# Kernel tuning notes

Hardware: AMD Instinct MI355X
Metric: run time of the kernel (lower is better)

Reference implementation:

```python
import jax, jax.numpy as jnp
import numpy as np


def squash(t, axis=0):
    # torch: norm over `axis` (dim removed), then norm^2 * t / ((1+norm^2)*norm),
    # broadcasting the reduced norm against t (right-aligned broadcast).
    norm = jnp.linalg.norm(t, axis=axis)
    return (norm ** 2) * t / ((1.0 + norm ** 2) * norm)


def setup_inputs() -> dict:
    key = jax.random.key(0)
    k1, k2 = jax.random.split(key)
    x = jax.random.normal(k1, (8, 16, 96, 96), dtype=jnp.float32)
    # (ker_h=5, ker_w=5, in_maps=16, num_atoms=8, out_maps=16)
    weights = jax.random.normal(k2, (5, 5, 16, 8, 16), dtype=jnp.float32)
    return {"x": x, "weights": weights, "num_routes": 3}


def reference(x, weights, num_routes):
    B, Cin, H, W = x.shape
    kh, kw, _, A, Cout = weights.shape

    # --- voting: zero-insertion (x2) + pad 2 + 5x5 sliding windows + einsum ---
    # torch builds a 2Hx2W zero-inserted tensor (trailing zero row/col), pads by 2,
    # then unfolds 5x5 patches at every position -> output spatial 2H x 2W and
    # contracts 'abcdef,efbhi->acdhi' (cross-correlation over kernel + in_maps).
    # This is exactly an lhs-dilated conv: dilation 2 gives size 2H-1, so pad
    # (2, 3) reproduces the torch layout (pad 2 each side of 2H incl. trailing zero).
    w = weights.reshape(kh, kw, Cin, A * Cout)  # HWIO
    out = jax.lax.conv_general_dilated(
        x, w,
        window_strides=(1, 1),
        padding=[(2, 3), (2, 3)],
        lhs_dilation=(2, 2),
        dimension_numbers=("NCHW", "HWIO", "NHWC"),
    )  # (B, 2H, 2W, A*Cout)
    votes = out.reshape(B, 2 * H, 2 * W, A, Cout)      # acdhi
    votes = jnp.transpose(votes, (0, 3, 4, 1, 2))      # (B, A, Cout, 2H, 2W) = abcde

    # --- dynamic routing (faithful, incl. softmax over the BATCH axis and the
    # logits = softmax(logits) reassignment before the additive update) ---
    logits = jnp.zeros((B, A, 2 * H, 2 * W), dtype=x.dtype)
    preds = None
    for _ in range(num_routes):
        logits = jax.nn.softmax(logits, axis=0)
        preds = jnp.einsum("abcde,abde->bcde", votes, logits)  # sum over batch
        preds = squash(preds, axis=0)                            # over num_atoms
        logits = logits + jnp.einsum("abcde,bcde->abde", votes, preds)
    return preds  # (A, Cout, 2H, 2W)
```

## Files before the change

kernel.cpp:

```cpp
#include <hip/hip_runtime.h>

#define XH 96
#define XW 96
#define CIN 16
#define NA 8
#define NC 16
#define OH 192
#define OW 192
#define WP 102
#define PADN (CIN * XH * WP * 8)

__global__ __launch_bounds__(256) void pad_x(const float* __restrict__ x,
                                             float* __restrict__ xp) {
  int idx = blockIdx.x * 256 + threadIdx.x;
  if (idx >= PADN) return;
  int b   = idx & 7;
  int t   = idx >> 3;
  int ixp = t % WP;
  int t2  = t / WP;
  int iy  = t2 % XH;
  int ci  = t2 / XH;
  int ix  = ixp - 1;
  float v = 0.f;
  if (ix >= 0 && ix < XW)
    v = x[((b * CIN + ci) * XH + iy) * XW + ix];
  xp[idx] = v;
}

__device__ __forceinline__ void route_pair(
    const float (&va)[8][2], const float (&vb)[8][2],
    int R, float (&qa)[2], float (&qb)[2])
{
  float lga[8], lgb[8];
#pragma unroll
  for (int b = 0; b < 8; ++b) { lga[b] = 0.f; lgb[b] = 0.f; }
#pragma unroll 1
  for (int r = 0; r < R; ++r) {
    float sla[8], slb[8];
    if (r == 0) {
#pragma unroll
      for (int b = 0; b < 8; ++b) { sla[b] = 0.125f; slb[b] = 0.125f; }
    } else {
      float ma = lga[0], mb = lgb[0];
#pragma unroll
      for (int b = 1; b < 8; ++b) { ma = fmaxf(ma, lga[b]); mb = fmaxf(mb, lgb[b]); }
      float sa = 0.f, sb = 0.f;
#pragma unroll
      for (int b = 0; b < 8; ++b) {
        sla[b] = __expf(lga[b] - ma); sa += sla[b];
        slb[b] = __expf(lgb[b] - mb); sb += slb[b];
      }
      const float ira = __builtin_amdgcn_rcpf(sa);
      const float irb = __builtin_amdgcn_rcpf(sb);
#pragma unroll
      for (int b = 0; b < 8; ++b) { sla[b] *= ira; slb[b] *= irb; }
    }

    qa[0] = 0.f; qa[1] = 0.f; qb[0] = 0.f; qb[1] = 0.f;
#pragma unroll
    for (int b = 0; b < 8; ++b) {
      qa[0] += va[b][0] * sla[b];  qa[1] += va[b][1] * sla[b];
      qb[0] += vb[b][0] * slb[b];  qb[1] += vb[b][1] * slb[b];
    }

#pragma unroll
    for (int i = 0; i < 2; ++i) {
      float na = qa[i] * qa[i], nb = qb[i] * qb[i];
      na += __shfl_xor(na, 8);  nb += __shfl_xor(nb, 8);
      na += __shfl_xor(na, 16); nb += __shfl_xor(nb, 16);
      na += __shfl_xor(na, 32); nb += __shfl_xor(nb, 32);
      qa[i] *= sqrtf(na) * __builtin_amdgcn_rcpf(1.f + na);
      qb[i] *= sqrtf(nb) * __builtin_amdgcn_rcpf(1.f + nb);
    }

    if (r + 1 < R) {
#pragma unroll
      for (int b = 0; b < 8; ++b) {
        float da = va[b][0] * qa[0] + va[b][1] * qa[1];
        float db = vb[b][0] * qb[0] + vb[b][1] * qb[1];
        da += __shfl_xor(da, 1);  db += __shfl_xor(db, 1);
        da += __shfl_xor(da, 2);  db += __shfl_xor(db, 2);
        da += __shfl_xor(da, 4);  db += __shfl_xor(db, 4);
        lga[b] = sla[b] + da;     lgb[b] = slb[b] + db;
      }
    }
  }
}

__global__ __launch_bounds__(256, 4) void upcaps_tr(
    const float* __restrict__ xp,
    const float* __restrict__ wts,
    const int* __restrict__ nroutes,
    float* __restrict__ out)
{
  __shared__ float lds_out[16 * 128];

  const int lane = threadIdx.x & 63;
  const int wid  = threadIdx.x >> 6;
  const int tile = blockIdx.x;
  const int oy   = tile / 12;
  const int xg   = (tile - oy * 12) * 16;
  const int pxb  = (wid & 1) + ((wid >> 1) << 3);
  const int oxw  = xg + pxb;
  const int a    = lane >> 3;
  const int cg   = lane & 7;
  const int e    = oxw & 1;
  const int ixp0 = __builtin_amdgcn_readfirstlane(((oxw - 2 + e) >> 1) + 1);
  const bool use_t2 = (__builtin_amdgcn_readfirstlane(e) == 0);
  const int wlane = a * NC + cg * 2;

  float acc[4][8][2];
#pragma unroll
  for (int j = 0; j < 4; ++j)
#pragma unroll
    for (int b = 0; b < 8; ++b) { acc[j][b][0] = 0.f; acc[j][b][1] = 0.f; }

  for (int ky = 0; ky < 5; ++ky) {
    const int py = oy - 2 + ky;
    if (py < 0 || py > 2 * XH - 2 || (py & 1)) continue;
    const int iy = py >> 1;
#pragma unroll 2
    for (int ci = 0; ci < CIN; ++ci) {
      const float* xrow = xp + ((ci * XH + iy) * WP + ixp0) * 8;
      float2 wv0, wv1, wv2;
      {
        const float* w0 = wts + ((ky * 5 + e)     * CIN + ci) * (NA * NC) + wlane;
        const float* w1 = wts + ((ky * 5 + e + 2) * CIN + ci) * (NA * NC) + wlane;
        wv0 = *(const float2*)w0;
        wv1 = *(const float2*)w1;
        wv2 = make_float2(0.f, 0.f);
        if (use_t2) {
          const float* w2 = wts + ((ky * 5 + 4) * CIN + ci) * (NA * NC) + wlane;
          wv2 = *(const float2*)w2;
        }
      }
#pragma unroll
      for (int ir = 0; ir < 6; ++ir) {
        if (ir == 5 && !use_t2) continue;
        const float4 xlo = *(const float4*)(xrow + ir * 8);
        const float4 xhi = *(const float4*)(xrow + ir * 8 + 4);
        const float xv[8] = {xlo.x, xlo.y, xlo.z, xlo.w,
                             xhi.x, xhi.y, xhi.z, xhi.w};
        if (ir <= 3) {
#pragma unroll
          for (int b = 0; b < 8; ++b) {
            acc[ir][b][0] += xv[b] * wv0.x;  acc[ir][b][1] += xv[b] * wv0.y;
          }
        }
        if (ir >= 1 && ir <= 4) {
#pragma unroll
          for (int b = 0; b < 8; ++b) {
            acc[ir-1][b][0] += xv[b] * wv1.x;  acc[ir-1][b][1] += xv[b] * wv1.y;
          }
        }
        if (ir >= 2 && use_t2) {
#pragma unroll
          for (int b = 0; b < 8; ++b) {
            acc[ir-2][b][0] += xv[b] * wv2.x;  acc[ir-2][b][1] += xv[b] * wv2.y;
          }
        }
      }
    }
  }

  const int R = nroutes[0];
  float q0[2], q1[2], q2[2], q3[2];
  route_pair(acc[0], acc[1], R, q0, q1);
  route_pair(acc[2], acc[3], R, q2, q3);

  const int lbase = a * NC + cg * 2;
  *(float2*)&lds_out[(pxb    ) * 128 + lbase] = make_float2(q0[0], q0[1]);
  *(float2*)&lds_out[(pxb + 2) * 128 + lbase] = make_float2(q1[0], q1[1]);
  *(float2*)&lds_out[(pxb + 4) * 128 + lbase] = make_float2(q2[0], q2[1]);
  *(float2*)&lds_out[(pxb + 6) * 128 + lbase] = make_float2(q3[0], q3[1]);
  __syncthreads();

  const int t = threadIdx.x;
  const int r = t >> 1, h = t & 1;
  float4 f0, f1;
  f0.x = lds_out[(h * 8 + 0) * 128 + r];
  f0.y = lds_out[(h * 8 + 1) * 128 + r];
  f0.z = lds_out[(h * 8 + 2) * 128 + r];
  f0.w = lds_out[(h * 8 + 3) * 128 + r];
  f1.x = lds_out[(h * 8 + 4) * 128 + r];
  f1.y = lds_out[(h * 8 + 5) * 128 + r];
  f1.z = lds_out[(h * 8 + 6) * 128 + r];
  f1.w = lds_out[(h * 8 + 7) * 128 + r];
  float* op = out + r * (OH * OW) + oy * OW + xg + h * 8;
  *(float4*)op       = f0;
  *(float4*)(op + 4) = f1;
}

extern "C" void kernel_launch(void* const* d_in, const int* in_sizes, int n_in,
                              void* d_out, int out_size, void* d_ws, size_t ws_size,
                              hipStream_t stream) {
  const float* x   = (const float*)d_in[0];
  const float* w   = (const float*)d_in[1];
  const int*   nr  = (const int*)d_in[2];
  float*       out = (float*)d_out;
  float*       xp  = (float*)d_ws;

  pad_x<<<(PADN + 255) / 256, 256, 0, stream>>>(x, xp);
  upcaps_tr<<<(OH * OW) / 16, 256, 0, stream>>>(xp, w, nr, out);
}
```

Baseline: 145.5 us.

## Stage input rows in LDS per tile and use packed float2 FMAs

```diff
diff --git a/kernel.cpp b/kernel.cpp
--- a/kernel.cpp
+++ b/kernel.cpp
@@ -1,4 +1,6 @@
 #include <hip/hip_runtime.h>
+
+typedef float v2f __attribute__((ext_vector_type(2)));
 
 #define XH 96
 #define XW 96
@@ -28,8 +30,7 @@
 }
 
 __device__ __forceinline__ void route_pair(
-    const float (&va)[8][2], const float (&vb)[8][2],
-    int R, float (&qa)[2], float (&qb)[2])
+    const v2f (&va)[8], const v2f (&vb)[8], int R, v2f& qa, v2f& qb)
 {
   float lga[8], lgb[8];
 #pragma unroll
@@ -56,28 +57,33 @@
       for (int b = 0; b < 8; ++b) { sla[b] *= ira; slb[b] *= irb; }
     }
 
-    qa[0] = 0.f; qa[1] = 0.f; qb[0] = 0.f; qb[1] = 0.f;
+    qa = (v2f){0.f, 0.f};  qb = (v2f){0.f, 0.f};
 #pragma unroll
     for (int b = 0; b < 8; ++b) {
-      qa[0] += va[b][0] * sla[b];  qa[1] += va[b][1] * sla[b];
-      qb[0] += vb[b][0] * slb[b];  qb[1] += vb[b][1] * slb[b];
-    }
-
-#pragma unroll
-    for (int i = 0; i < 2; ++i) {
-      float na = qa[i] * qa[i], nb = qb[i] * qb[i];
-      na += __shfl_xor(na, 8);  nb += __shfl_xor(nb, 8);
-      na += __shfl_xor(na, 16); nb += __shfl_xor(nb, 16);
-      na += __shfl_xor(na, 32); nb += __shfl_xor(nb, 32);
-      qa[i] *= sqrtf(na) * __builtin_amdgcn_rcpf(1.f + na);
-      qb[i] *= sqrtf(nb) * __builtin_amdgcn_rcpf(1.f + nb);
+      qa = __builtin_elementwise_fma((v2f){sla[b], sla[b]}, va[b], qa);
+      qb = __builtin_elementwise_fma((v2f){slb[b], slb[b]}, vb[b], qb);
+    }
+
+    {
+      float na0 = qa.x * qa.x, na1 = qa.y * qa.y;
+      float nb0 = qb.x * qb.x, nb1 = qb.y * qb.y;
+      na0 += __shfl_xor(na0, 8);  na1 += __shfl_xor(na1, 8);
+      nb0 += __shfl_xor(nb0, 8);  nb1 += __shfl_xor(nb1, 8);
+      na0 += __shfl_xor(na0, 16); na1 += __shfl_xor(na1, 16);
+      nb0 += __shfl_xor(nb0, 16); nb1 += __shfl_xor(nb1, 16);
+      na0 += __shfl_xor(na0, 32); na1 += __shfl_xor(na1, 32);
+      nb0 += __shfl_xor(nb0, 32); nb1 += __shfl_xor(nb1, 32);
+      qa.x *= sqrtf(na0) * __builtin_amdgcn_rcpf(1.f + na0);
+      qa.y *= sqrtf(na1) * __builtin_amdgcn_rcpf(1.f + na1);
+      qb.x *= sqrtf(nb0) * __builtin_amdgcn_rcpf(1.f + nb0);
+      qb.y *= sqrtf(nb1) * __builtin_amdgcn_rcpf(1.f + nb1);
     }
 
     if (r + 1 < R) {
 #pragma unroll
       for (int b = 0; b < 8; ++b) {
-        float da = va[b][0] * qa[0] + va[b][1] * qa[1];
-        float db = vb[b][0] * qb[0] + vb[b][1] * qb[1];
+        float da = fmaf(va[b].x, qa.x, va[b].y * qa.y);
+        float db = fmaf(vb[b].x, qb.x, vb[b].y * qb.y);
         da += __shfl_xor(da, 1);  db += __shfl_xor(db, 1);
         da += __shfl_xor(da, 2);  db += __shfl_xor(db, 2);
         da += __shfl_xor(da, 4);  db += __shfl_xor(db, 4);
@@ -87,76 +93,92 @@
   }
 }
 
-__global__ __launch_bounds__(256, 4) void upcaps_tr(
+__global__ __launch_bounds__(256, 4) void upcaps_tr2(
     const float* __restrict__ xp,
     const float* __restrict__ wts,
     const int* __restrict__ nroutes,
     float* __restrict__ out)
 {
-  __shared__ float lds_out[16 * 128];
+  __shared__ float smem[3840];
 
   const int lane = threadIdx.x & 63;
   const int wid  = threadIdx.x >> 6;
   const int tile = blockIdx.x;
   const int oy   = tile / 12;
   const int xg   = (tile - oy * 12) * 16;
+  const int xgh  = xg >> 1;
+  const int kyBase = oy & 1;
+
+  for (int s = threadIdx.x; s < 480; s += 256) {
+    const int col = s % 10;
+    const int t   = s / 10;
+    const int kyI = t % 3;
+    const int ci  = t / 3;
+    const int ky  = kyBase + 2 * kyI;
+    const int py  = oy - 2 + ky;
+    if (ky <= 4 && py >= 0 && py <= 2 * XH - 2) {
+      const int iy = py >> 1;
+      const float4* src = (const float4*)(xp + ((ci * XH + iy) * WP + (xgh + col)) * 8);
+      float4* dst = (float4*)&smem[((ci * 3 + kyI) * 10 + col) * 8];
+      dst[0] = src[0];
+      dst[1] = src[1];
+    }
+  }
+  __syncthreads();
+
   const int pxb  = (wid & 1) + ((wid >> 1) << 3);
-  const int oxw  = xg + pxb;
   const int a    = lane >> 3;
   const int cg   = lane & 7;
-  const int e    = oxw & 1;
-  const int ixp0 = __builtin_amdgcn_readfirstlane(((oxw - 2 + e) >> 1) + 1);
-  const bool use_t2 = (__builtin_amdgcn_readfirstlane(e) == 0);
+  const int e    = pxb & 1;
+  const int wcol0 = (wid & 1) + (wid >> 1) * 4;
+  const bool use_t2 = (e == 0);
   const int wlane = a * NC + cg * 2;
 
-  float acc[4][8][2];
+  v2f acc[4][8];
 #pragma unroll
   for (int j = 0; j < 4; ++j)
 #pragma unroll
-    for (int b = 0; b < 8; ++b) { acc[j][b][0] = 0.f; acc[j][b][1] = 0.f; }
-
-  for (int ky = 0; ky < 5; ++ky) {
+    for (int b = 0; b < 8; ++b) acc[j][b] = (v2f){0.f, 0.f};
+
+  for (int kyI = 0; kyI < 3; ++kyI) {
+    const int ky = kyBase + 2 * kyI;
     const int py = oy - 2 + ky;
-    if (py < 0 || py > 2 * XH - 2 || (py & 1)) continue;
-    const int iy = py >> 1;
+    if (ky > 4 || py < 0 || py > 2 * XH - 2) continue;
+    const float* xbase = &smem[(kyI * 10 + wcol0) * 8];
+    const float* wk = wts + (ky * 5 + e) * (CIN * NA * NC) + wlane;
 #pragma unroll 2
     for (int ci = 0; ci < CIN; ++ci) {
-      const float* xrow = xp + ((ci * XH + iy) * WP + ixp0) * 8;
-      float2 wv0, wv1, wv2;
-      {
-        const float* w0 = wts + ((ky * 5 + e)     * CIN + ci) * (NA * NC) + wlane;
-        const float* w1 = wts + ((ky * 5 + e + 2) * CIN + ci) * (NA * NC) + wlane;
-        wv0 = *(const float2*)w0;
-        wv1 = *(const float2*)w1;
-        wv2 = make_float2(0.f, 0.f);
-        if (use_t2) {
-          const float* w2 = wts + ((ky * 5 + 4) * CIN + ci) * (NA * NC) + wlane;
-          wv2 = *(const float2*)w2;
-        }
-      }
+      const v2f cw0 = *(const v2f*)(wk + ci * (NA * NC));
+      const v2f cw1 = *(const v2f*)(wk + 2 * (CIN * NA * NC) + ci * (NA * NC));
+      v2f cw2 = (v2f){0.f, 0.f};
+      if (use_t2) cw2 = *(const v2f*)(wk + 4 * (CIN * NA * NC) + ci * (NA * NC));
+      const float* xci = xbase + ci * 240;
 #pragma unroll
       for (int ir = 0; ir < 6; ++ir) {
         if (ir == 5 && !use_t2) continue;
-        const float4 xlo = *(const float4*)(xrow + ir * 8);
-        const float4 xhi = *(const float4*)(xrow + ir * 8 + 4);
+        const float4 xlo = *(const float4*)(xci + ir * 8);
+        const float4 xhi = *(const float4*)(xci + ir * 8 + 4);
         const float xv[8] = {xlo.x, xlo.y, xlo.z, xlo.w,
                              xhi.x, xhi.y, xhi.z, xhi.w};
         if (ir <= 3) {
 #pragma unroll
           for (int b = 0; b < 8; ++b) {
-            acc[ir][b][0] += xv[b] * wv0.x;  acc[ir][b][1] += xv[b] * wv0.y;
+            const v2f xs = (v2f){xv[b], xv[b]};
+            acc[ir][b] = __builtin_elementwise_fma(xs, cw0, acc[ir][b]);
           }
         }
         if (ir >= 1 && ir <= 4) {
 #pragma unroll
           for (int b = 0; b < 8; ++b) {
-            acc[ir-1][b][0] += xv[b] * wv1.x;  acc[ir-1][b][1] += xv[b] * wv1.y;
+            const v2f xs = (v2f){xv[b], xv[b]};
+            acc[ir - 1][b] = __builtin_elementwise_fma(xs, cw1, acc[ir - 1][b]);
           }
         }
         if (ir >= 2 && use_t2) {
 #pragma unroll
           for (int b = 0; b < 8; ++b) {
-            acc[ir-2][b][0] += xv[b] * wv2.x;  acc[ir-2][b][1] += xv[b] * wv2.y;
+            const v2f xs = (v2f){xv[b], xv[b]};
+            acc[ir - 2][b] = __builtin_elementwise_fma(xs, cw2, acc[ir - 2][b]);
           }
         }
       }
@@ -164,15 +186,17 @@
   }
 
   const int R = nroutes[0];
-  float q0[2], q1[2], q2[2], q3[2];
+  v2f q0, q1, q2, q3;
   route_pair(acc[0], acc[1], R, q0, q1);
   route_pair(acc[2], acc[3], R, q2, q3);
 
+  __syncthreads();
+  float* lds_out = smem;
   const int lbase = a * NC + cg * 2;
-  *(float2*)&lds_out[(pxb    ) * 128 + lbase] = make_float2(q0[0], q0[1]);
-  *(float2*)&lds_out[(pxb + 2) * 128 + lbase] = make_float2(q1[0], q1[1]);
-  *(float2*)&lds_out[(pxb + 4) * 128 + lbase] = make_float2(q2[0], q2[1]);
-  *(float2*)&lds_out[(pxb + 6) * 128 + lbase] = make_float2(q3[0], q3[1]);
+  *(v2f*)&lds_out[(pxb    ) * 128 + lbase] = q0;
+  *(v2f*)&lds_out[(pxb + 2) * 128 + lbase] = q1;
+  *(v2f*)&lds_out[(pxb + 4) * 128 + lbase] = q2;
+  *(v2f*)&lds_out[(pxb + 6) * 128 + lbase] = q3;
   __syncthreads();
 
   const int t = threadIdx.x;
@@ -201,5 +225,5 @@
   float*       xp  = (float*)d_ws;
 
   pad_x<<<(PADN + 255) / 256, 256, 0, stream>>>(x, xp);
-  upcaps_tr<<<(OH * OW) / 16, 256, 0, stream>>>(xp, w, nr, out);
-}
+  upcaps_tr2<<<(OH * OW) / 16, 256, 0, stream>>>(xp, w, nr, out);
+}
```

New measurement: 166.9 us. 14.7% more time.
